# Kernel tuning notes

Measured on AMD Instinct MI355X. Metric: run time of the kernel, lower is better.

The kernel has to match this reference:

```python
import jax, jax.numpy as jnp
import numpy as np

C = 2       # channels
F_IN = 1024  # n_fft//2
F = 512      # n_fft//4 (transformer features)
L = 12       # num layers
E = 4        # expansion
H = 8        # num heads
EPS = 1e-5


def mcl(x, pw, dw=None):
    # x: [b,c,f_in,w]; pw: [c,f_out,f_in]; dw: [c_out,c_in]
    if pw is not None:
        x = jnp.einsum('bciw,coi->bcow', x, pw)
    if dw is not None:
        x = jnp.einsum('bcfw,dc->bdfw', x, dw)
    return x


def sq_relu(x):
    return jnp.square(jax.nn.relu(x))


def frame_norm(x, w, b):
    # x: [b,c,f,w] -> layernorm over f (applied as torch does on transposed view)
    xt = jnp.swapaxes(x, 2, 3)  # [b,c,w,f]
    mu = xt.mean(-1, keepdims=True)
    var = xt.var(-1, keepdims=True)
    y = (xt - mu) * jax.lax.rsqrt(var + EPS) * w + b  # w,b: [c,1,f]
    return jnp.swapaxes(y, 2, 3)


def rope(t):
    # t: [b,c,H,w,dh]; interleaved RoPE (lucidrains rotary-embedding-torch)
    dh = t.shape[-1]
    w = t.shape[-2]
    inv = 1.0 / (10000.0 ** (jnp.arange(0, dh, 2, dtype=jnp.float32) / dh))
    freqs = jnp.arange(w, dtype=jnp.float32)[:, None] * inv[None, :]  # [w, dh/2]
    freqs = jnp.repeat(freqs, 2, axis=-1)  # [w, dh]
    cos, sin = jnp.cos(freqs), jnp.sin(freqs)
    t1, t2 = t[..., 0::2], t[..., 1::2]
    rot = jnp.stack([-t2, t1], axis=-1).reshape(t.shape)
    return t * cos + rot * sin


def attention(x, q_pw, q_dw, k_pw, k_dw, v_pw, v_dw, o_pw):
    b, c, f, w = x.shape
    dh = f // H
    def heads(t):  # [b,c,f,w] -> [b,c,H,w,dh]
        return jnp.swapaxes(t, 2, 3).reshape(b, c, w, H, dh).transpose(0, 1, 3, 2, 4)
    q = rope(heads(mcl(x, q_pw, q_dw)))
    k = rope(heads(mcl(x, k_pw, k_dw)))
    v = heads(mcl(x, v_pw, v_dw))
    # note: original scales by 1/sqrt(features), not 1/sqrt(head_dim)
    s = jnp.einsum('bchqd,bchkd->bchqk', q.astype(jnp.float32), k.astype(jnp.float32)) / jnp.sqrt(jnp.float32(f))
    p = jax.nn.softmax(s, axis=-1)
    a = jnp.einsum('bchqk,bchkd->bchqd', p, v.astype(jnp.float32))
    a = a.transpose(0, 1, 3, 2, 4).reshape(b, c, w, f)  # [b,c,w,f]
    a = jnp.swapaxes(a, 2, 3)  # [b,c,f,w]
    return mcl(a, o_pw, None)


def frame_block(x, l1_pw, l1_dw, l2_pw, l2_dw, id_pw, id_dw):
    z = mcl(sq_relu(mcl(x, l1_pw, l1_dw)), l2_pw, l2_dw)
    return mcl(x, id_pw, id_dw) + z


def reference(x, e1_pw, e1_dw, e2_pw, e2_dw, ei_pw, ei_dw,
              n1_w, n1_b, q_pw, q_dw, k_pw, k_dw, v_pw, v_dw, o_pw,
              n2_w, n2_b, f1_pw, f2_pw,
              d1_pw, d1_dw, d2_pw, d2_dw, di_pw, di_dw):
    e = frame_block(x, e1_pw, e1_dw, e2_pw, e2_dw, ei_pw, ei_dw)  # [b,c,512,w]
    for i in range(L):
        h = frame_norm(e, n1_w[i], n1_b[i])
        h = attention(h, q_pw[i], q_dw[i], k_pw[i], k_dw[i], v_pw[i], v_dw[i], o_pw[i])
        e = e + h
        h = frame_norm(e, n2_w[i], n2_b[i])
        h = mcl(sq_relu(mcl(h, f1_pw[i], None)), f2_pw[i], None)
        e = e + h
    d = frame_block(e, d1_pw, d1_dw, d2_pw, d2_dw, di_pw, di_dw)  # [b,c,1024,w]
    return d


def setup_inputs() -> dict:
    key = jax.random.key(0)
    ks = iter(jax.random.split(key, 64))
    def u(shape, fan_in):
        b = 1.0 / np.sqrt(fan_in)
        return jax.random.uniform(next(ks), shape, jnp.float32, -b, b)
    inp = {}
    inp['x'] = jax.random.normal(next(ks), (2, C, F_IN, 512), jnp.float32)
    # encoder (in_f=1024 -> out_f=512), depthwise
    inp['e1_pw'] = u((C, F, F_IN), F_IN); inp['e1_dw'] = u((C, C), C)
    inp['e2_pw'] = u((C, F, F), F);       inp['e2_dw'] = u((C, C), C)
    inp['ei_pw'] = u((C, F, F_IN), F_IN); inp['ei_dw'] = u((C, C), C)
    # transformer layers (stacked over L)
    inp['n1_w'] = jnp.ones((L, C, 1, F), jnp.float32)
    inp['n1_b'] = jnp.zeros((L, C, 1, F), jnp.float32)
    inp['q_pw'] = u((L, C, F, F), F); inp['q_dw'] = u((L, C, C), C)
    inp['k_pw'] = u((L, C, F, F), F); inp['k_dw'] = u((L, C, C), C)
    inp['v_pw'] = u((L, C, F, F), F); inp['v_dw'] = u((L, C, C), C)
    inp['o_pw'] = u((L, C, F, F), F)
    inp['n2_w'] = jnp.ones((L, C, 1, F), jnp.float32)
    inp['n2_b'] = jnp.zeros((L, C, 1, F), jnp.float32)
    inp['f1_pw'] = u((L, C, F * E, F), F)
    inp['f2_pw'] = u((L, C, F, F * E), F * E)
    # decoder (in_f=512 -> out_f=1024), depthwise
    inp['d1_pw'] = u((C, F_IN, F), F);       inp['d1_dw'] = u((C, C), C)
    inp['d2_pw'] = u((C, F_IN, F_IN), F_IN); inp['d2_dw'] = u((C, C), C)
    inp['di_pw'] = u((C, F_IN, F), F);       inp['di_dw'] = u((C, C), C)
    return inp
```

## Files before the change

kernel.cpp:

```cpp
#include <hip/hip_runtime.h>
#include <math.h>


typedef short s16x8 __attribute__((ext_vector_type(8)));
typedef float f32x4 __attribute__((ext_vector_type(4)));
typedef unsigned short u16;
#define MFMA(a,b,c) __builtin_amdgcn_mfma_f32_16x16x32_bf16(a,b,c,0,0,0)

__device__ __forceinline__ float4 ld4(const float* p){ return *(const float4*)p; }
__device__ __forceinline__ void st4(float* p, float4 v){ *(float4*)p = v; }
__device__ __forceinline__ float4 f4fma2(float a, float4 x, float b, float4 y){
  float4 r; r.x=a*x.x+b*y.x; r.y=a*x.y+b*y.y; r.z=a*x.z+b*y.z; r.w=a*x.w+b*y.w; return r;
}
__device__ __forceinline__ float4 f4add(float4 a, float4 b){
  float4 r; r.x=a.x+b.x; r.y=a.y+b.y; r.z=a.z+b.z; r.w=a.w+b.w; return r;
}
__device__ __forceinline__ float4 f4sqrelu(float4 a){
  float4 r;
  r.x = a.x>0.f ? a.x*a.x : 0.f; r.y = a.y>0.f ? a.y*a.y : 0.f;
  r.z = a.z>0.f ? a.z*a.z : 0.f; r.w = a.w>0.f ? a.w*a.w : 0.f;
  return r;
}

__device__ __forceinline__ void cvt8(float4 a, float4 b, s16x8* hi, s16x8* lo){
  union { s16x8 v; unsigned short u[8]; } H, L;
  float f[8] = {a.x,a.y,a.z,a.w,b.x,b.y,b.z,b.w};
  #pragma unroll
  for (int j=0;j<8;j++){
    unsigned u = __float_as_uint(f[j]);
    H.u[j] = (unsigned short)(u>>16);
    float hf = __uint_as_float(u & 0xffff0000u);
    float lf = f[j] - hf;
    L.u[j] = (unsigned short)(__float_as_uint(lf)>>16);
  }
  *hi = H.v; *lo = L.v;
}

__device__ __forceinline__ void cvt4(float4 a, ushort4* hi, ushort4* lo){
  unsigned short hh[4], ll[4];
  float f[4] = {a.x,a.y,a.z,a.w};
  #pragma unroll
  for (int j=0;j<4;j++){
    unsigned u = __float_as_uint(f[j]);
    hh[j] = (unsigned short)(u>>16);
    float hf = __uint_as_float(u & 0xffff0000u);
    ll[j] = (unsigned short)(__float_as_uint(f[j]-hf)>>16);
  }
  ushort4 H, L;
  H.x=hh[0];H.y=hh[1];H.z=hh[2];H.w=hh[3];
  L.x=ll[0];L.y=ll[1];L.z=ll[2];L.w=ll[3];
  *hi=H; *lo=L;
}

__device__ __forceinline__ void gl16(const void* g, void* l){
  __builtin_amdgcn_global_load_lds((const __attribute__((address_space(1))) void*)g,
                                   (__attribute__((address_space(3))) void*)l, 16, 0, 0);
}

__global__ __launch_bounds__(256) void rope_tab_k(float* __restrict__ cosT, float* __restrict__ sinT){
  int idx = blockIdx.x*256 + threadIdx.x;
  int w = idx >> 5, j = idx & 31;
  float th = (float)w * powf(10000.f, -(float)(2*j)/64.f);
  cosT[idx] = cosf(th);
  sinT[idx] = sinf(th);
}

template<int VAR>
__global__ __launch_bounds__(256) void wcvt_k(
    const float* __restrict__ s0, const float* __restrict__ s1, const float* __restrict__ s2,
    const float* __restrict__ s3, const float* __restrict__ s4, const float* __restrict__ s5,
    u16* __restrict__ H, u16* __restrict__ L)
{
  const int seg = blockIdx.y;
  const float* src; int n; size_t off;
  if (VAR == 0){
    if      (seg==0){ src=s0; n= 524288; off=0; }
    else if (seg==1){ src=s1; n= 524288; off= 524288; }
    else if (seg==2){ src=s2; n= 524288; off=1048576; }
    else if (seg==3){ src=s3; n= 524288; off=1572864; }
    else if (seg==4){ src=s4; n=2097152; off=2097152; }
    else            { src=s5; n=2097152; off=4194304; }
  } else if (VAR == 1){
    if      (seg==0){ src=s0; n=1048576; off=0; }
    else if (seg==1){ src=s1; n= 524288; off=1048576; }
    else            { src=s2; n=1048576; off=1572864; }
  } else {
    if      (seg==0){ src=s0; n=1048576; off=0; }
    else if (seg==1){ src=s1; n=2097152; off=1048576; }
    else            { src=s2; n=1048576; off=3145728; }
  }
  const int idx = blockIdx.x*256 + threadIdx.x;
  if (idx*8 >= n) return;
  float4 a = ld4(src + (size_t)idx*8);
  float4 b = ld4(src + (size_t)idx*8 + 4);
  s16x8 h,l; cvt8(a,b,&h,&l);
  *(s16x8*)&H[off + (size_t)idx*8] = h;
  *(s16x8*)&L[off + (size_t)idx*8] = l;
}

__global__ __launch_bounds__(256) void cvt_k(const float* __restrict__ X,
                                             u16* __restrict__ H, u16* __restrict__ L){
  const int idx = blockIdx.x*256 + threadIdx.x;
  float4 a = ld4(X + (size_t)idx*8);
  float4 b = ld4(X + (size_t)idx*8 + 4);
  s16x8 h,l; cvt8(a,b,&h,&l);
  *(s16x8*)&H[(size_t)idx*8] = h;
  *(s16x8*)&L[(size_t)idx*8] = l;
}

__global__ __launch_bounds__(256) void statsnorm_k(
    const float* __restrict__ E, const float* __restrict__ G, const float* __restrict__ Bt,
    u16* __restrict__ BH, u16* __restrict__ BL)
{
  int row = (blockIdx.x<<2) + (threadIdx.x>>6);
  int lane = threadIdx.x & 63;
  int c = (row >> 9) & 1;
  const float* p = E + (size_t)row*512 + (lane<<3);
  float4 a = ld4(p), b = ld4(p+4);
  float s = a.x+a.y+a.z+a.w + b.x+b.y+b.z+b.w;
  float q = a.x*a.x+a.y*a.y+a.z*a.z+a.w*a.w + b.x*b.x+b.y*b.y+b.z*b.z+b.w*b.w;
  #pragma unroll
  for (int off=32; off; off>>=1){ s += __shfl_xor(s,off); q += __shfl_xor(q,off); }
  float mu = s*(1.f/512.f);
  float rs = rsqrtf(q*(1.f/512.f) - mu*mu + 1e-5f);
  const float* gp = G  + c*512 + (lane<<3);
  const float* bp = Bt + c*512 + (lane<<3);
  float4 g0 = ld4(gp), g1 = ld4(gp+4), b0 = ld4(bp), b1 = ld4(bp+4);
  a.x = (a.x-mu)*rs*g0.x + b0.x; a.y = (a.y-mu)*rs*g0.y + b0.y;
  a.z = (a.z-mu)*rs*g0.z + b0.z; a.w = (a.w-mu)*rs*g0.w + b0.w;
  b.x = (b.x-mu)*rs*g1.x + b1.x; b.y = (b.y-mu)*rs*g1.y + b1.y;
  b.z = (b.z-mu)*rs*g1.z + b1.z; b.w = (b.w-mu)*rs*g1.w + b1.w;
  s16x8 h,l; cvt8(a,b,&h,&l);
  size_t o = (size_t)row*512 + (lane<<3);
  *(s16x8*)&BH[o] = h; *(s16x8*)&BL[o] = l;
}

template<int EPI, bool ACC, bool FUSE3>
__global__ __launch_bounds__(256) void mm_k(
    const u16* __restrict__ AH_, const u16* __restrict__ AL_,
    const u16* __restrict__ BH_, const u16* __restrict__ BL_,
    float* __restrict__ Y_, u16* __restrict__ YH_, u16* __restrict__ YL_,
    int M, int K)
{
  const int z = blockIdx.z;
  const int bc = FUSE3 ? (z & 3) : z;
  const int c = bc & 1;
  const size_t aoff = (size_t)c*M*K + (FUSE3 ? (size_t)(z>>2)*524288 : (size_t)0);
  const u16* AHp = AH_ + aoff;
  const u16* ALp = AL_ + aoff;
  const u16* BHp = BH_ + (size_t)bc*512*K;
  const u16* BLp = BL_ + (size_t)bc*512*K;

  const int n0 = blockIdx.x << 6, m0 = blockIdx.y << 6;
  const int t = threadIdx.x;
  const int lane = t & 63, wv = t >> 6;

  __shared__ __align__(16) unsigned char smem[65536];
  u16* sm = (u16*)smem;

  const int Rb  = wv*16 + (lane>>3);
  const int sc8 = ((lane & 7) ^ (Rb & 7)) << 3;
  const u16* gA0 = AHp + (size_t)(m0+Rb)*K + sc8;
  const u16* gA1 = ALp + (size_t)(m0+Rb)*K + sc8;
  const u16* gB0 = BHp + (size_t)(n0+Rb)*K + sc8;
  const u16* gB1 = BLp + (size_t)(n0+Rb)*K + sc8;
  const size_t r8 = (size_t)8*K;

  auto stage = [&](int half, int kt){
    u16* lb = sm + (half<<14) + (wv<<10);
    const int k64 = kt << 6;
    gl16(gA0 + k64,      lb);
    gl16(gA0 + r8 + k64, lb + 512);
    gl16(gA1 + k64,      lb + 4096);
    gl16(gA1 + r8 + k64, lb + 4608);
    gl16(gB0 + k64,      lb + 8192);
    gl16(gB0 + r8 + k64, lb + 8704);
    gl16(gB1 + k64,      lb + 12288);
    gl16(gB1 + r8 + k64, lb + 12800);
  };

  const int fr = lane & 15, fq = lane >> 4;
  const int mq = (wv >> 1) << 5, nq = (wv & 1) << 5;
  const int ra0 = (mq + fr)<<6, ra1 = (mq + 16 + fr)<<6;
  const int rb0 = (nq + fr)<<6, rb1 = (nq + 16 + fr)<<6;
  const int frx = fr & 7;

  f32x4 acc00 = {0,0,0,0}, acc01 = {0,0,0,0}, acc10 = {0,0,0,0}, acc11 = {0,0,0,0};
  const int NT = K >> 6;

  stage(0, 0);
  __syncthreads();
  for (int kt = 0; kt < NT; kt++){
    if (kt + 1 < NT) stage((kt+1)&1, kt+1);
    const u16* cb = sm + ((kt&1)<<14);
    #pragma unroll
    for (int ks = 0; ks < 64; ks += 32){
      const int cs = ((((ks>>3) + fq) ^ frx) << 3);
      s16x8 aH0 = *(const s16x8*)&cb[ra0 + cs];
      s16x8 aH1 = *(const s16x8*)&cb[ra1 + cs];
      s16x8 aL0 = *(const s16x8*)&cb[4096 + ra0 + cs];
      s16x8 aL1 = *(const s16x8*)&cb[4096 + ra1 + cs];
      s16x8 bH0 = *(const s16x8*)&cb[8192 + rb0 + cs];
      s16x8 bH1 = *(const s16x8*)&cb[8192 + rb1 + cs];
      s16x8 bL0 = *(const s16x8*)&cb[12288 + rb0 + cs];
      s16x8 bL1 = *(const s16x8*)&cb[12288 + rb1 + cs];
      acc00 = MFMA(aH0,bH0,acc00); acc00 = MFMA(aH0,bL0,acc00); acc00 = MFMA(aL0,bH0,acc00);
      acc01 = MFMA(aH0,bH1,acc01); acc01 = MFMA(aH0,bL1,acc01); acc01 = MFMA(aL0,bH1,acc01);
      acc10 = MFMA(aH1,bH0,acc10); acc10 = MFMA(aH1,bL0,acc10); acc10 = MFMA(aL1,bH0,acc10);
      acc11 = MFMA(aH1,bH1,acc11); acc11 = MFMA(aH1,bL1,acc11); acc11 = MFMA(aL1,bH1,acc11);
    }
    __syncthreads();
  }

  float* Yt = (float*)smem;
  #pragma unroll
  for (int i=0;i<4;i++){
    Yt[(nq      + fr)*72 + mq      + fq*4 + i] = acc00[i];
    Yt[(nq + 16 + fr)*72 + mq      + fq*4 + i] = acc01[i];
    Yt[(nq      + fr)*72 + mq + 16 + fq*4 + i] = acc10[i];
    Yt[(nq + 16 + fr)*72 + mq + 16 + fq*4 + i] = acc11[i];
  }
  __syncthreads();
  const int sr = t >> 2, scB = (t & 3) << 4;
  if (EPI == 1){
    float4 r0 = f4sqrelu(*(float4*)&Yt[sr*72 + scB]);
    float4 r1 = f4sqrelu(*(float4*)&Yt[sr*72 + scB + 4]);
    float4 r2 = f4sqrelu(*(float4*)&Yt[sr*72 + scB + 8]);
    float4 r3 = f4sqrelu(*(float4*)&Yt[sr*72 + scB + 12]);
    u16* YH = YH_ + (size_t)bc*512*M;
    u16* YL = YL_ + (size_t)bc*512*M;
    size_t base = (size_t)(n0 + sr)*M + m0 + scB;
    s16x8 h,l;
    cvt8(r0,r1,&h,&l); *(s16x8*)&YH[base]   = h; *(s16x8*)&YL[base]   = l;
    cvt8(r2,r3,&h,&l); *(s16x8*)&YH[base+8] = h; *(s16x8*)&YL[base+8] = l;
  } else {
    float* Y = Y_ + (FUSE3 ? (size_t)(z>>2)*1048576 : (size_t)0) + (size_t)bc*512*M;
    #pragma unroll
    for (int i=0;i<4;i++){
      float4 r = *(float4*)&Yt[sr*72 + scB + i*4];
      float* dst = &Y[(size_t)(n0 + sr)*M + m0 + scB + i*4];
      if (ACC) r = f4add(r, ld4(dst));
      st4(dst, r);
    }
  }
}

template<int MODE>
__global__ __launch_bounds__(256) void dwmix_k(
    const float* __restrict__ T, const float* __restrict__ dwp,
    const float* __restrict__ Z, float* __restrict__ O,
    u16* __restrict__ OH, u16* __restrict__ OL, int F)
{
  int idx = blockIdx.x*256 + threadIdx.x;
  int perb = F << 7;
  int b = idx / perb; int rem = idx - b*perb;
  size_t i0 = ((size_t)(b*2) * F)*512 + (size_t)rem*4;
  size_t i1 = i0 + (size_t)F*512;
  float4 t0 = ld4(T + i0), t1 = ld4(T + i1);
  float d00 = dwp[0], d01 = dwp[1], d10 = dwp[2], d11 = dwp[3];
  float4 o0 = f4fma2(d00, t0, d01, t1);
  float4 o1 = f4fma2(d10, t0, d11, t1);
  if (MODE == 1){
    o0 = f4sqrelu(o0); o1 = f4sqrelu(o1);
    ushort4 h,l;
    cvt4(o0,&h,&l); *(ushort4*)&OH[i0] = h; *(ushort4*)&OL[i0] = l;
    cvt4(o1,&h,&l); *(ushort4*)&OH[i1] = h; *(ushort4*)&OL[i1] = l;
  } else if (MODE == 2){
    o0 = f4add(o0, ld4(Z + i0)); o1 = f4add(o1, ld4(Z + i1));
    st4(O + i0, o0); st4(O + i1, o1);
  } else {
    st4(O + i0, o0); st4(O + i1, o1);
  }
}

__global__ __launch_bounds__(256) void qkv_post_k(
    const float* __restrict__ QY, const float* __restrict__ qdw,
    const float* __restrict__ kdw, const float* __restrict__ vdw,
    float* __restrict__ qB, float* __restrict__ kB, float* __restrict__ vB,
    const float* __restrict__ cosT, const float* __restrict__ sinT)
{
  int p = blockIdx.y;
  const float* T = QY + (size_t)p*1048576;
  const float* dwp = (p==0) ? qdw : ((p==1) ? kdw : vdw);
  float* O = (p==0) ? qB : ((p==1) ? kB : vB);
  int idx = blockIdx.x*256 + threadIdx.x;
  int b = idx >> 16; int rem = idx & 65535;
  int w = rem >> 7; int f = (rem & 127) << 2;
  size_t i0 = ((size_t)(b*2)*512 + w)*512 + f;
  size_t i1 = i0 + 262144;
  float4 t0 = ld4(T+i0), t1 = ld4(T+i1);
  float d00 = dwp[0], d01 = dwp[1], d10 = dwp[2], d11 = dwp[3];
  float4 o0 = f4fma2(d00, t0, d01, t1);
  float4 o1 = f4fma2(d10, t0, d11, t1);
  if (p < 2){
    int j = (f & 63) >> 1;
    float c0 = cosT[w*32 + j], c1 = cosT[w*32 + j + 1];
    float s0 = sinT[w*32 + j], s1 = sinT[w*32 + j + 1];
    float4 r0, r1;
    r0.x = o0.x*c0 - o0.y*s0;  r0.y = o0.y*c0 + o0.x*s0;
    r0.z = o0.z*c1 - o0.w*s1;  r0.w = o0.w*c1 + o0.z*s1;
    r1.x = o1.x*c0 - o1.y*s0;  r1.y = o1.y*c0 + o1.x*s0;
    r1.z = o1.z*c1 - o1.w*s1;  r1.w = o1.w*c1 + o1.z*s1;
    o0 = r0; o1 = r1;
  }
  st4(O + i0, o0);
  st4(O + i1, o1);
}

__global__ __launch_bounds__(256) void transpose_x_k(const float* __restrict__ X,
                                                     u16* __restrict__ XH, u16* __restrict__ XL){
  __shared__ float T[64][68];
  int w0 = blockIdx.x << 6, f0 = blockIdx.y << 6, bc = blockIdx.z;
  int r = threadIdx.x >> 2, c4 = (threadIdx.x & 3) << 4;
  const float* src = X + ((size_t)bc*1024 + f0 + r)*512 + w0 + c4;
  #pragma unroll
  for (int i=0;i<4;i++) st4(&T[r][c4 + i*4], ld4(src + i*4));
  __syncthreads();
  size_t base = ((size_t)bc*512 + w0 + r)*1024 + f0 + c4;
  #pragma unroll
  for (int i=0;i<2;i++){
    float4 v0, v1;
    v0.x = T[c4+i*8+0][r]; v0.y = T[c4+i*8+1][r]; v0.z = T[c4+i*8+2][r]; v0.w = T[c4+i*8+3][r];
    v1.x = T[c4+i*8+4][r]; v1.y = T[c4+i*8+5][r]; v1.z = T[c4+i*8+6][r]; v1.w = T[c4+i*8+7][r];
    s16x8 h,l; cvt8(v0,v1,&h,&l);
    *(s16x8*)&XH[base + i*8] = h;
    *(s16x8*)&XL[base + i*8] = l;
  }
}

__global__ __launch_bounds__(256) void out_t_k(const float* __restrict__ T_, const float* __restrict__ dwp,
                                               const float* __restrict__ Z, float* __restrict__ O){
  __shared__ float T0[64][68], T1[64][68];
  int w0 = blockIdx.x << 6, f0 = blockIdx.y << 6, b = blockIdx.z;
  int r = threadIdx.x >> 2, c4 = (threadIdx.x & 3) << 4;
  size_t base0 = ((size_t)(b*2)*512 + w0 + r)*1024 + f0 + c4;
  size_t base1 = base0 + 524288;
  float d00 = dwp[0], d01 = dwp[1], d10 = dwp[2], d11 = dwp[3];
  #pragma unroll
  for (int i=0;i<4;i++){
    float4 t0 = ld4(T_+base0+i*4), t1 = ld4(T_+base1+i*4);
    float4 z0 = ld4(Z+base0+i*4),  z1 = ld4(Z+base1+i*4);
    st4(&T0[r][c4+i*4], f4add(f4fma2(d00,t0,d01,t1), z0));
    st4(&T1[r][c4+i*4], f4add(f4fma2(d10,t0,d11,t1), z1));
  }
  __syncthreads();
  size_t ob0 = ((size_t)(b*2)*1024 + f0 + r)*512 + w0 + c4;
  size_t ob1 = ob0 + 524288;
  #pragma unroll
  for (int i=0;i<4;i++){
    float4 v0, v1;
    v0.x=T0[c4+i*4+0][r]; v0.y=T0[c4+i*4+1][r]; v0.z=T0[c4+i*4+2][r]; v0.w=T0[c4+i*4+3][r];
    v1.x=T1[c4+i*4+0][r]; v1.y=T1[c4+i*4+1][r]; v1.z=T1[c4+i*4+2][r]; v1.w=T1[c4+i*4+3][r];
    st4(O+ob0+i*4, v0);
    st4(O+ob1+i*4, v1);
  }
}

__global__ __launch_bounds__(256) void attn_k(
    const float* __restrict__ Q, const float* __restrict__ K,
    const float* __restrict__ V, u16* __restrict__ aoH, u16* __restrict__ aoL)
{
  const int q0 = blockIdx.x << 6;
  const int hc = blockIdx.y << 6;
  const int bc = blockIdx.z;
  const size_t cb = (size_t)bc*262144;
  const float* Qp = Q + cb;
  const float* Kp = K + cb;
  const float* Vp = V + cb;

  __shared__ __align__(16) unsigned short QH[64*72];
  __shared__ __align__(16) unsigned short QL[64*72];
  __shared__ __align__(16) unsigned short TH[64*72];
  __shared__ __align__(16) unsigned short TL[64*72];
  __shared__ float St[64*68];
  __shared__ float mL[64], lL[64], aLs[64];

  const int t = threadIdx.x, lane = t & 63, wv = t >> 6;
  const int fr = lane & 15, fq = lane >> 4;
  const int mq = wv << 4;

  {
    int r = t >> 2, c16 = (t & 3) << 4;
    const float* src = Qp + (size_t)(q0 + r)*512 + hc + c16;
    float4 v0 = ld4(src), v1 = ld4(src+4), v2 = ld4(src+8), v3 = ld4(src+12);
    s16x8 h,l;
    cvt8(v0,v1,&h,&l); *(s16x8*)&QH[r*72+c16]   = h; *(s16x8*)&QL[r*72+c16]   = l;
    cvt8(v2,v3,&h,&l); *(s16x8*)&QH[r*72+c16+8] = h; *(s16x8*)&QL[r*72+c16+8] = l;
  }
  if (t < 64){ mL[t] = -1e30f; lL[t] = 0.f; }

  f32x4 oA[4] = {{0,0,0,0},{0,0,0,0},{0,0,0,0},{0,0,0,0}};
  const float sc = 0.044194173824159216f;

  for (int k0 = 0; k0 < 512; k0 += 64){
    __syncthreads();
    {
      int r = t >> 2, c16 = (t & 3) << 4;
      const float* src = Kp + (size_t)(k0 + r)*512 + hc + c16;
      float4 v0 = ld4(src), v1 = ld4(src+4), v2 = ld4(src+8), v3 = ld4(src+12);
      s16x8 h,l;
      cvt8(v0,v1,&h,&l); *(s16x8*)&TH[r*72+c16]   = h; *(s16x8*)&TL[r*72+c16]   = l;
      cvt8(v2,v3,&h,&l); *(s16x8*)&TH[r*72+c16+8] = h; *(s16x8*)&TL[r*72+c16+8] = l;
    }
    __syncthreads();
    {
      f32x4 sA[4] = {{0,0,0,0},{0,0,0,0},{0,0,0,0},{0,0,0,0}};
      #pragma unroll
      for (int ks = 0; ks < 64; ks += 32){
        int ao = (mq + fr)*72 + ks + fq*8;
        s16x8 aH = *(const s16x8*)&QH[ao];
        s16x8 aLo = *(const s16x8*)&QL[ao];
        #pragma unroll
        for (int nt = 0; nt < 4; nt++){
          int bo = ((nt<<4) + fr)*72 + ks + fq*8;
          s16x8 bH = *(const s16x8*)&TH[bo];
          s16x8 bLo = *(const s16x8*)&TL[bo];
          sA[nt] = MFMA(aH,bH,sA[nt]);
          sA[nt] = MFMA(aLo,bH,sA[nt]);
          sA[nt] = MFMA(aH,bLo,sA[nt]);
        }
      }
      #pragma unroll
      for (int nt = 0; nt < 4; nt++)
        #pragma unroll
        for (int i = 0; i < 4; i++)
          St[(mq + fq*4 + i)*68 + (nt<<4) + fr] = sA[nt][i]*sc;
    }
    __syncthreads();
    {
      int r = t >> 2, sub = t & 3;
      float* row = &St[r*68 + (sub << 4)];
      float4 x0 = ((float4*)row)[0], x1 = ((float4*)row)[1];
      float4 x2 = ((float4*)row)[2], x3 = ((float4*)row)[3];
      float mx = fmaxf(fmaxf(fmaxf(x0.x,x0.y),fmaxf(x0.z,x0.w)),
                       fmaxf(fmaxf(x1.x,x1.y),fmaxf(x1.z,x1.w)));
      mx = fmaxf(mx, fmaxf(fmaxf(fmaxf(x2.x,x2.y),fmaxf(x2.z,x2.w)),
                           fmaxf(fmaxf(x3.x,x3.y),fmaxf(x3.z,x3.w))));
      mx = fmaxf(mx, __shfl_xor(mx, 1));
      mx = fmaxf(mx, __shfl_xor(mx, 2));
      float mo = mL[r];
      float mn = fmaxf(mo, mx);
      float al = __expf(mo - mn);
      x0.x=__expf(x0.x-mn); x0.y=__expf(x0.y-mn); x0.z=__expf(x0.z-mn); x0.w=__expf(x0.w-mn);
      x1.x=__expf(x1.x-mn); x1.y=__expf(x1.y-mn); x1.z=__expf(x1.z-mn); x1.w=__expf(x1.w-mn);
      x2.x=__expf(x2.x-mn); x2.y=__expf(x2.y-mn); x2.z=__expf(x2.z-mn); x2.w=__expf(x2.w-mn);
      x3.x=__expf(x3.x-mn); x3.y=__expf(x3.y-mn); x3.z=__expf(x3.z-mn); x3.w=__expf(x3.w-mn);
      float sm = (x0.x+x0.y+x0.z+x0.w) + (x1.x+x1.y+x1.z+x1.w)
               + (x2.x+x2.y+x2.z+x2.w) + (x3.x+x3.y+x3.z+x3.w);
      sm += __shfl_xor(sm, 1);
      sm += __shfl_xor(sm, 2);
      ((float4*)row)[0]=x0; ((float4*)row)[1]=x1; ((float4*)row)[2]=x2; ((float4*)row)[3]=x3;
      if (sub == 0){ mL[r] = mn; lL[r] = lL[r]*al + sm; aLs[r] = al; }
    }
    {
      int c16 = wv << 4;
      const float* src = Vp + (size_t)(k0 + lane)*512 + hc + c16;
      #pragma unroll
      for (int jj = 0; jj < 16; jj += 4){
        float4 v = ld4(src + jj);
        float f[4] = {v.x, v.y, v.z, v.w};
        #pragma unroll
        for (int e = 0; e < 4; e++){
          unsigned u = __float_as_uint(f[e]);
          TH[(c16+jj+e)*72 + lane] = (unsigned short)(u>>16);
          float hf = __uint_as_float(u & 0xffff0000u);
          TL[(c16+jj+e)*72 + lane] = (unsigned short)(__float_as_uint(f[e]-hf)>>16);
        }
      }
    }
    __syncthreads();
    {
      float a0 = aLs[mq + fq*4 + 0], a1 = aLs[mq + fq*4 + 1];
      float a2 = aLs[mq + fq*4 + 2], a3 = aLs[mq + fq*4 + 3];
      #pragma unroll
      for (int nt = 0; nt < 4; nt++){
        oA[nt][0] *= a0; oA[nt][1] *= a1; oA[nt][2] *= a2; oA[nt][3] *= a3;
      }
      #pragma unroll
      for (int ks = 0; ks < 64; ks += 32){
        const float* pr = &St[(mq + fr)*68 + ks + fq*8];
        float4 p0 = ld4(pr), p1 = ld4(pr+4);
        s16x8 pH, pL;
        cvt8(p0, p1, &pH, &pL);
        #pragma unroll
        for (int nt = 0; nt < 4; nt++){
          int bo = ((nt<<4) + fr)*72 + ks + fq*8;
          s16x8 bH = *(const s16x8*)&TH[bo];
          s16x8 bLo = *(const s16x8*)&TL[bo];
          oA[nt] = MFMA(pH,bH,oA[nt]);
          oA[nt] = MFMA(pL,bH,oA[nt]);
          oA[nt] = MFMA(pH,bLo,oA[nt]);
        }
      }
    }
  }
  {
    float i0 = 1.f / lL[mq + fq*4 + 0], i1 = 1.f / lL[mq + fq*4 + 1];
    float i2 = 1.f / lL[mq + fq*4 + 2], i3 = 1.f / lL[mq + fq*4 + 3];
    #pragma unroll
    for (int nt = 0; nt < 4; nt++){
      St[(mq + fq*4 + 0)*68 + (nt<<4) + fr] = oA[nt][0]*i0;
      St[(mq + fq*4 + 1)*68 + (nt<<4) + fr] = oA[nt][1]*i1;
      St[(mq + fq*4 + 2)*68 + (nt<<4) + fr] = oA[nt][2]*i2;
      St[(mq + fq*4 + 3)*68 + (nt<<4) + fr] = oA[nt][3]*i3;
    }
  }
  __syncthreads();
  {
    int r = t >> 2, c16 = (t & 3) << 4;
    size_t base = cb + (size_t)(q0 + r)*512 + hc + c16;
    float4 v0 = *(float4*)&St[r*68 + c16];
    float4 v1 = *(float4*)&St[r*68 + c16 + 4];
    float4 v2 = *(float4*)&St[r*68 + c16 + 8];
    float4 v3 = *(float4*)&St[r*68 + c16 + 12];
    s16x8 h,l;
    cvt8(v0,v1,&h,&l); *(s16x8*)&aoH[base]   = h; *(s16x8*)&aoL[base]   = l;
    cvt8(v2,v3,&h,&l); *(s16x8*)&aoH[base+8] = h; *(s16x8*)&aoL[base+8] = l;
  }
}

extern "C" void kernel_launch(void* const* d_in, const int* in_sizes, int n_in,
                              void* d_out, int out_size, void* d_ws, size_t ws_size,
                              hipStream_t stream) {
  (void)in_sizes; (void)n_in; (void)out_size; (void)ws_size;
  const float* x     = (const float*)d_in[0];
  const float* e1_pw = (const float*)d_in[1];
  const float* e1_dw = (const float*)d_in[2];
  const float* e2_pw = (const float*)d_in[3];
  const float* e2_dw = (const float*)d_in[4];
  const float* ei_pw = (const float*)d_in[5];
  const float* ei_dw = (const float*)d_in[6];
  const float* n1_w  = (const float*)d_in[7];
  const float* n1_b  = (const float*)d_in[8];
  const float* q_pw  = (const float*)d_in[9];
  const float* q_dw  = (const float*)d_in[10];
  const float* k_pw  = (const float*)d_in[11];
  const float* k_dw  = (const float*)d_in[12];
  const float* v_pw  = (const float*)d_in[13];
  const float* v_dw  = (const float*)d_in[14];
  const float* o_pw  = (const float*)d_in[15];
  const float* n2_w  = (const float*)d_in[16];
  const float* n2_b  = (const float*)d_in[17];
  const float* f1_pw = (const float*)d_in[18];
  const float* f2_pw = (const float*)d_in[19];
  const float* d1_pw = (const float*)d_in[20];
  const float* d1_dw = (const float*)d_in[21];
  const float* d2_pw = (const float*)d_in[22];
  const float* d2_dw = (const float*)d_in[23];
  const float* di_pw = (const float*)d_in[24];
  const float* di_dw = (const float*)d_in[25];

  float* W    = (float*)d_ws;
  float* bufA = W;
  float* eB   = W + 3145728;
  float* qB   = W + 4194304;
  float* kB   = W + 5242880;
  float* vB   = W + 6291456;
  float* Zbuf = W + 7340032;
  float* cosT = W + 9437184;
  float* sinT = W + 9453568;
  u16* P   = (u16*)(W + 9469952);
  u16* xTH = P;
  u16* xTL = xTH + 2097152;
  u16* nBH = xTL + 2097152;
  u16* nBL = nBH + 1048576;
  u16* aoH = nBL + 1048576;
  u16* aoL = aoH + 1048576;
  u16* f2H = aoL + 1048576;
  u16* f2L = f2H + 4194304;
  u16* sqH = f2L + 4194304;
  u16* sqL = sqH + 2097152;
  u16* ePH = sqL + 2097152;
  u16* ePL = ePH + 1048576;
  u16* LWH = ePL + 1048576;
  u16* LWL = LWH + 6291456;
  float* os = (float*)d_out;

  const dim3 blk(256);

  rope_tab_k<<<64, blk, 0, stream>>>(cosT, sinT);
  transpose_x_k<<<dim3(8,16,4), blk, 0, stream>>>(x, xTH, xTL);

  wcvt_k<1><<<dim3(512,3), blk, 0, stream>>>(e1_pw, e2_pw, ei_pw, nullptr, nullptr, nullptr, LWH, LWL);
  mm_k<0,false,false><<<dim3(8,8,4), blk, 0, stream>>>(LWH, LWL, xTH, xTL, bufA, nullptr, nullptr, 512, 1024);
  dwmix_k<1><<<512, blk, 0, stream>>>(bufA, e1_dw, nullptr, nullptr, sqH, sqL, 512);
  mm_k<0,false,false><<<dim3(8,8,4), blk, 0, stream>>>(LWH+1048576, LWL+1048576, sqH, sqL, bufA, nullptr, nullptr, 512, 512);
  dwmix_k<0><<<512, blk, 0, stream>>>(bufA, e2_dw, nullptr, Zbuf, nullptr, nullptr, 512);
  mm_k<0,false,false><<<dim3(8,8,4), blk, 0, stream>>>(LWH+1572864, LWL+1572864, xTH, xTL, bufA, nullptr, nullptr, 512, 1024);
  dwmix_k<2><<<512, blk, 0, stream>>>(bufA, ei_dw, Zbuf, eB, nullptr, nullptr, 512);

  for (int i = 0; i < 12; i++){
    const float* n1w = n1_w + i*1024; const float* n1b = n1_b + i*1024;
    const float* n2w = n2_w + i*1024; const float* n2b = n2_b + i*1024;
    size_t qo = (size_t)i*524288, fo = (size_t)i*2097152;

    wcvt_k<0><<<dim3(1024,6), blk, 0, stream>>>(q_pw+qo, k_pw+qo, v_pw+qo, o_pw+qo, f1_pw+fo, f2_pw+fo, LWH, LWL);
    statsnorm_k<<<512, blk, 0, stream>>>(eB, n1w, n1b, nBH, nBL);
    mm_k<0,false,true><<<dim3(8,8,12), blk, 0, stream>>>(LWH, LWL, nBH, nBL, bufA, nullptr, nullptr, 512, 512);
    qkv_post_k<<<dim3(512,3), blk, 0, stream>>>(bufA, q_dw+i*4, k_dw+i*4, v_dw+i*4, qB, kB, vB, cosT, sinT);
    attn_k<<<dim3(8,8,4), blk, 0, stream>>>(qB, kB, vB, aoH, aoL);
    mm_k<0,true,false><<<dim3(8,8,4), blk, 0, stream>>>(LWH+1572864, LWL+1572864, aoH, aoL, eB, nullptr, nullptr, 512, 512);

    statsnorm_k<<<512, blk, 0, stream>>>(eB, n2w, n2b, nBH, nBL);
    mm_k<1,false,false><<<dim3(8,32,4), blk, 0, stream>>>(LWH+2097152, LWL+2097152, nBH, nBL, nullptr, f2H, f2L, 2048, 512);
    mm_k<0,true,false><<<dim3(8,8,4), blk, 0, stream>>>(LWH+4194304, LWL+4194304, f2H, f2L, eB, nullptr, nullptr, 512, 2048);
  }

  wcvt_k<2><<<dim3(1024,3), blk, 0, stream>>>(d1_pw, d2_pw, di_pw, nullptr, nullptr, nullptr, LWH, LWL);
  cvt_k<<<512, blk, 0, stream>>>(eB, ePH, ePL);
  mm_k<0,false,false><<<dim3(8,16,4), blk, 0, stream>>>(LWH, LWL, ePH, ePL, bufA, nullptr, nullptr, 1024, 512);
  dwmix_k<1><<<1024, blk, 0, stream>>>(bufA, d1_dw, nullptr, nullptr, sqH, sqL, 1024);
  mm_k<0,false,false><<<dim3(8,16,4), blk, 0, stream>>>(LWH+1048576, LWL+1048576, sqH, sqL, bufA, nullptr, nullptr, 1024, 1024);
  dwmix_k<0><<<1024, blk, 0, stream>>>(bufA, d2_dw, nullptr, Zbuf, nullptr, nullptr, 1024);
  mm_k<0,false,false><<<dim3(8,16,4), blk, 0, stream>>>(LWH+3145728, LWL+3145728, ePH, ePL, bufA, nullptr, nullptr, 1024, 512);
  out_t_k<<<dim3(8,16,2), blk, 0, stream>>>(bufA, di_dw, Zbuf, os);
}
```

Baseline: 1.962 ms.

## Pre-split QKV to bf16 hi/lo and pipeline attention K loads asynchronously

qkv_post_k now writes Q, K and V as bf16 hi/lo pairs, so the attention kernel no longer converts fp32 inside its loop. attn_k loads Q and K tiles directly into LDS with swizzled global_load_lds, double-buffers K across key tiles, and prefetches V into registers, holding Q fragments in registers throughout. The GEMM main loop and attention replace __syncthreads with explicit vmcnt/lgkmcnt waits plus raw barriers, so the next tile's prefetch overlaps compute. The hand-written waitcnt counts must match the number of outstanding loads exactly, otherwise a stale-data race appears.

Result: faster. 1.858 ms (-5.3%).

```diff
diff --git a/kernel.cpp b/kernel.cpp
--- a/kernel.cpp
+++ b/kernel.cpp
@@ -55,6 +55,15 @@
 __device__ __forceinline__ void gl16(const void* g, void* l){
   __builtin_amdgcn_global_load_lds((const __attribute__((address_space(1))) void*)g,
                                    (__attribute__((address_space(3))) void*)l, 16, 0, 0);
+}
+
+__device__ __forceinline__ void wait_vm8(){ asm volatile("s_waitcnt vmcnt(8)" ::: "memory"); }
+__device__ __forceinline__ void wait_vm4(){ asm volatile("s_waitcnt vmcnt(4)" ::: "memory"); }
+__device__ __forceinline__ void wait_vm0(){ asm volatile("s_waitcnt vmcnt(0)" ::: "memory"); }
+__device__ __forceinline__ void wait_lgkm0(){ asm volatile("s_waitcnt lgkmcnt(0)" ::: "memory"); }
+__device__ __forceinline__ void barrier_raw(){
+  __builtin_amdgcn_s_barrier();
+  __builtin_amdgcn_sched_barrier(0);
 }
 
 __global__ __launch_bounds__(256) void rope_tab_k(float* __restrict__ cosT, float* __restrict__ sinT){
@@ -189,9 +198,11 @@
   const int NT = K >> 6;
 
   stage(0, 0);
-  __syncthreads();
   for (int kt = 0; kt < NT; kt++){
-    if (kt + 1 < NT) stage((kt+1)&1, kt+1);
+    const bool pf = (kt + 1 < NT);
+    if (pf) stage((kt+1)&1, kt+1);
+    if (pf) wait_vm8(); else wait_vm0();
+    barrier_raw();
     const u16* cb = sm + ((kt&1)<<14);
     #pragma unroll
     for (int ks = 0; ks < 64; ks += 32){
@@ -209,7 +220,8 @@
       acc10 = MFMA(aH1,bH0,acc10); acc10 = MFMA(aH1,bL0,acc10); acc10 = MFMA(aL1,bH0,acc10);
       acc11 = MFMA(aH1,bH1,acc11); acc11 = MFMA(aH1,bL1,acc11); acc11 = MFMA(aL1,bH1,acc11);
     }
-    __syncthreads();
+    wait_lgkm0();
+    barrier_raw();
   }
 
   float* Yt = (float*)smem;
@@ -276,13 +288,16 @@
 __global__ __launch_bounds__(256) void qkv_post_k(
     const float* __restrict__ QY, const float* __restrict__ qdw,
     const float* __restrict__ kdw, const float* __restrict__ vdw,
-    float* __restrict__ qB, float* __restrict__ kB, float* __restrict__ vB,
+    u16* __restrict__ qHp, u16* __restrict__ qLp,
+    u16* __restrict__ kHp, u16* __restrict__ kLp,
+    u16* __restrict__ vHp, u16* __restrict__ vLp,
     const float* __restrict__ cosT, const float* __restrict__ sinT)
 {
   int p = blockIdx.y;
   const float* T = QY + (size_t)p*1048576;
   const float* dwp = (p==0) ? qdw : ((p==1) ? kdw : vdw);
-  float* O = (p==0) ? qB : ((p==1) ? kB : vB);
+  u16* OH = (p==0) ? qHp : ((p==1) ? kHp : vHp);
+  u16* OL = (p==0) ? qLp : ((p==1) ? kLp : vLp);
   int idx = blockIdx.x*256 + threadIdx.x;
   int b = idx >> 16; int rem = idx & 65535;
   int w = rem >> 7; int f = (rem & 127) << 2;
@@ -303,8 +318,9 @@
     r1.z = o1.z*c1 - o1.w*s1;  r1.w = o1.w*c1 + o1.z*s1;
     o0 = r0; o1 = r1;
   }
-  st4(O + i0, o0);
-  st4(O + i1, o1);
+  ushort4 h,l;
+  cvt4(o0,&h,&l); *(ushort4*)&OH[i0] = h; *(ushort4*)&OL[i0] = l;
+  cvt4(o1,&h,&l); *(ushort4*)&OH[i1] = h; *(ushort4*)&OL[i1] = l;
 }
 
 __global__ __launch_bounds__(256) void transpose_x_k(const float* __restrict__ X,
@@ -357,64 +373,94 @@
 }
 
 __global__ __launch_bounds__(256) void attn_k(
-    const float* __restrict__ Q, const float* __restrict__ K,
-    const float* __restrict__ V, u16* __restrict__ aoH, u16* __restrict__ aoL)
+    const u16* __restrict__ qHp, const u16* __restrict__ qLp,
+    const u16* __restrict__ kHp, const u16* __restrict__ kLp,
+    const u16* __restrict__ vHp, const u16* __restrict__ vLp,
+    u16* __restrict__ aoH, u16* __restrict__ aoL)
 {
   const int q0 = blockIdx.x << 6;
   const int hc = blockIdx.y << 6;
   const int bc = blockIdx.z;
   const size_t cb = (size_t)bc*262144;
-  const float* Qp = Q + cb;
-  const float* Kp = K + cb;
-  const float* Vp = V + cb;
-
-  __shared__ __align__(16) unsigned short QH[64*72];
-  __shared__ __align__(16) unsigned short QL[64*72];
-  __shared__ __align__(16) unsigned short TH[64*72];
-  __shared__ __align__(16) unsigned short TL[64*72];
+  const u16* Qh = qHp + cb; const u16* Ql = qLp + cb;
+  const u16* Kh = kHp + cb; const u16* Kl = kLp + cb;
+  const u16* Vh = vHp + cb; const u16* Vl = vLp + cb;
+
+  __shared__ __align__(16) u16 QHs[4096], QLs[4096];
+  __shared__ __align__(16) u16 KHs[8192], KLs[8192];
+  __shared__ __align__(16) u16 TH[4608], TL[4608];
   __shared__ float St[64*68];
   __shared__ float mL[64], lL[64], aLs[64];
 
   const int t = threadIdx.x, lane = t & 63, wv = t >> 6;
   const int fr = lane & 15, fq = lane >> 4;
   const int mq = wv << 4;
+  const int frx = fr & 7;
+
+  const int sR  = lane >> 3;
+  const int sCh = ((lane & 7) ^ (sR & 7)) << 3;
+  const int wr  = wv*16 + sR;
 
   {
-    int r = t >> 2, c16 = (t & 3) << 4;
-    const float* src = Qp + (size_t)(q0 + r)*512 + hc + c16;
-    float4 v0 = ld4(src), v1 = ld4(src+4), v2 = ld4(src+8), v3 = ld4(src+12);
-    s16x8 h,l;
-    cvt8(v0,v1,&h,&l); *(s16x8*)&QH[r*72+c16]   = h; *(s16x8*)&QL[r*72+c16]   = l;
-    cvt8(v2,v3,&h,&l); *(s16x8*)&QH[r*72+c16+8] = h; *(s16x8*)&QL[r*72+c16+8] = l;
+    const u16* s0 = Qh + (size_t)(q0 + wr)*512 + hc + sCh;
+    u16* d0 = QHs + (wv<<10);
+    gl16(s0, d0); gl16(s0 + 8*512, d0 + 512);
+    const u16* s1 = Ql + (size_t)(q0 + wr)*512 + hc + sCh;
+    u16* d1 = QLs + (wv<<10);
+    gl16(s1, d1); gl16(s1 + 8*512, d1 + 512);
+    const u16* s2 = Kh + (size_t)wr*512 + hc + sCh;
+    u16* d2 = KHs + (wv<<10);
+    gl16(s2, d2); gl16(s2 + 8*512, d2 + 512);
+    const u16* s3 = Kl + (size_t)wr*512 + hc + sCh;
+    u16* d3 = KLs + (wv<<10);
+    gl16(s3, d3); gl16(s3 + 8*512, d3 + 512);
   }
   if (t < 64){ mL[t] = -1e30f; lL[t] = 0.f; }
+  wait_vm4();
+  barrier_raw();
+
+  s16x8 qh[2], ql[2];
+  #pragma unroll
+  for (int ksi = 0; ksi < 2; ksi++){
+    int cs = (((ksi<<2) + fq) ^ frx) << 3;
+    qh[ksi] = *(const s16x8*)&QHs[((mq+fr)<<6) + cs];
+    ql[ksi] = *(const s16x8*)&QLs[((mq+fr)<<6) + cs];
+  }
 
   f32x4 oA[4] = {{0,0,0,0},{0,0,0,0},{0,0,0,0},{0,0,0,0}};
   const float sc = 0.044194173824159216f;
 
-  for (int k0 = 0; k0 < 512; k0 += 64){
-    __syncthreads();
+  for (int kt = 0; kt < 8; kt++){
+    const int k0 = kt << 6;
+    const u16* vsh = Vh + (size_t)(k0 + lane)*512 + hc + (wv<<4);
+    const u16* vsl = Vl + (size_t)(k0 + lane)*512 + hc + (wv<<4);
+    s16x8 vh0 = *(const s16x8*)vsh;
+    s16x8 vh1 = *(const s16x8*)(vsh + 8);
+    s16x8 vl0 = *(const s16x8*)vsl;
+    s16x8 vl1 = *(const s16x8*)(vsl + 8);
+    if (kt < 7){
+      const u16* s2 = Kh + (size_t)((kt+1)*64 + wr)*512 + hc + sCh;
+      u16* d2 = KHs + (((kt+1)&1)<<12) + (wv<<10);
+      gl16(s2, d2); gl16(s2 + 8*512, d2 + 512);
+      const u16* s3 = Kl + (size_t)((kt+1)*64 + wr)*512 + hc + sCh;
+      u16* d3 = KLs + (((kt+1)&1)<<12) + (wv<<10);
+      gl16(s3, d3); gl16(s3 + 8*512, d3 + 512);
+    }
+    wait_lgkm0();
+    if (kt < 7) wait_vm8(); else wait_vm4();
+    barrier_raw();
     {
-      int r = t >> 2, c16 = (t & 3) << 4;
-      const float* src = Kp + (size_t)(k0 + r)*512 + hc + c16;
-      float4 v0 = ld4(src), v1 = ld4(src+4), v2 = ld4(src+8), v3 = ld4(src+12);
-      s16x8 h,l;
-      cvt8(v0,v1,&h,&l); *(s16x8*)&TH[r*72+c16]   = h; *(s16x8*)&TL[r*72+c16]   = l;
-      cvt8(v2,v3,&h,&l); *(s16x8*)&TH[r*72+c16+8] = h; *(s16x8*)&TL[r*72+c16+8] = l;
-    }
-    __syncthreads();
-    {
+      const int kbuf = (kt&1)<<12;
       f32x4 sA[4] = {{0,0,0,0},{0,0,0,0},{0,0,0,0},{0,0,0,0}};
       #pragma unroll
-      for (int ks = 0; ks < 64; ks += 32){
-        int ao = (mq + fr)*72 + ks + fq*8;
-        s16x8 aH = *(const s16x8*)&QH[ao];
-        s16x8 aLo = *(const s16x8*)&QL[ao];
+      for (int ksi = 0; ksi < 2; ksi++){
+        int cs = (((ksi<<2) + fq) ^ frx) << 3;
+        s16x8 aH = qh[ksi], aLo = ql[ksi];
         #pragma unroll
         for (int nt = 0; nt < 4; nt++){
-          int bo = ((nt<<4) + fr)*72 + ks + fq*8;
-          s16x8 bH = *(const s16x8*)&TH[bo];
-          s16x8 bLo = *(const s16x8*)&TL[bo];
+          int bo = kbuf + (((nt<<4) + fr)<<6) + cs;
+          s16x8 bH  = *(const s16x8*)&KHs[bo];
+          s16x8 bLo = *(const s16x8*)&KLs[bo];
           sA[nt] = MFMA(aH,bH,sA[nt]);
           sA[nt] = MFMA(aLo,bH,sA[nt]);
           sA[nt] = MFMA(aH,bLo,sA[nt]);
@@ -426,7 +472,8 @@
         for (int i = 0; i < 4; i++)
           St[(mq + fq*4 + i)*68 + (nt<<4) + fr] = sA[nt][i]*sc;
     }
-    __syncthreads();
+    wait_lgkm0();
+    barrier_raw();
     {
       int r = t >> 2, sub = t & 3;
       float* row = &St[r*68 + (sub << 4)];
@@ -454,21 +501,18 @@
     }
     {
       int c16 = wv << 4;
-      const float* src = Vp + (size_t)(k0 + lane)*512 + hc + c16;
+      union { s16x8 v; u16 u[8]; } a0,a1,b0,b1;
+      a0.v = vh0; a1.v = vh1; b0.v = vl0; b1.v = vl1;
       #pragma unroll
-      for (int jj = 0; jj < 16; jj += 4){
-        float4 v = ld4(src + jj);
-        float f[4] = {v.x, v.y, v.z, v.w};
-        #pragma unroll
-        for (int e = 0; e < 4; e++){
-          unsigned u = __float_as_uint(f[e]);
-          TH[(c16+jj+e)*72 + lane] = (unsigned short)(u>>16);
-          float hf = __uint_as_float(u & 0xffff0000u);
-          TL[(c16+jj+e)*72 + lane] = (unsigned short)(__float_as_uint(f[e]-hf)>>16);
-        }
+      for (int e=0;e<8;e++){
+        TH[(c16+e)*72 + lane]   = a0.u[e];
+        TL[(c16+e)*72 + lane]   = b0.u[e];
+        TH[(c16+8+e)*72 + lane] = a1.u[e];
+        TL[(c16+8+e)*72 + lane] = b1.u[e];
       }
     }
-    __syncthreads();
+    wait_lgkm0();
+    barrier_raw();
     {
       float a0 = aLs[mq + fq*4 + 0], a1 = aLs[mq + fq*4 + 1];
       float a2 = aLs[mq + fq*4 + 2], a3 = aLs[mq + fq*4 + 3];
@@ -485,7 +529,7 @@
         #pragma unroll
         for (int nt = 0; nt < 4; nt++){
           int bo = ((nt<<4) + fr)*72 + ks + fq*8;
-          s16x8 bH = *(const s16x8*)&TH[bo];
+          s16x8 bH  = *(const s16x8*)&TH[bo];
           s16x8 bLo = *(const s16x8*)&TL[bo];
           oA[nt] = MFMA(pH,bH,oA[nt]);
           oA[nt] = MFMA(pL,bH,oA[nt]);
@@ -553,9 +597,13 @@
   float* W    = (float*)d_ws;
   float* bufA = W;
   float* eB   = W + 3145728;
-  float* qB   = W + 4194304;
-  float* kB   = W + 5242880;
-  float* vB   = W + 6291456;
+  u16* qkvP = (u16*)(W + 4194304);
+  u16* qHp = qkvP;
+  u16* qLp = qHp + 1048576;
+  u16* kHp = qLp + 1048576;
+  u16* kLp = kHp + 1048576;
+  u16* vHp = kLp + 1048576;
+  u16* vLp = vHp + 1048576;
   float* Zbuf = W + 7340032;
   float* cosT = W + 9437184;
   float* sinT = W + 9453568;
@@ -597,8 +645,9 @@
     wcvt_k<0><<<dim3(1024,6), blk, 0, stream>>>(q_pw+qo, k_pw+qo, v_pw+qo, o_pw+qo, f1_pw+fo, f2_pw+fo, LWH, LWL);
     statsnorm_k<<<512, blk, 0, stream>>>(eB, n1w, n1b, nBH, nBL);
     mm_k<0,false,true><<<dim3(8,8,12), blk, 0, stream>>>(LWH, LWL, nBH, nBL, bufA, nullptr, nullptr, 512, 512);
-    qkv_post_k<<<dim3(512,3), blk, 0, stream>>>(bufA, q_dw+i*4, k_dw+i*4, v_dw+i*4, qB, kB, vB, cosT, sinT);
-    attn_k<<<dim3(8,8,4), blk, 0, stream>>>(qB, kB, vB, aoH, aoL);
+    qkv_post_k<<<dim3(512,3), blk, 0, stream>>>(bufA, q_dw+i*4, k_dw+i*4, v_dw+i*4,
+                                                qHp, qLp, kHp, kLp, vHp, vLp, cosT, sinT);
+    attn_k<<<dim3(8,8,4), blk, 0, stream>>>(qHp, qLp, kHp, kLp, vHp, vLp, aoH, aoL);
     mm_k<0,true,false><<<dim3(8,8,4), blk, 0, stream>>>(LWH+1572864, LWL+1572864, aoH, aoL, eB, nullptr, nullptr, 512, 512);
 
     statsnorm_k<<<512, blk, 0, stream>>>(eB, n2w, n2b, nBH, nBL);
```
